# Optimization experiments

Measured on AMD Instinct MI355X. Metric: run time of the kernel, lower is better.

The kernel has to match this reference:

```python
import jax, jax.numpy as jnp
import numpy as np

ALPHA = 0.2  # LeakyReLU negative slope
MASK_VAL = -9e15


def setup_inputs() -> dict:
    key = jax.random.key(0)
    k1, k2, k3 = jax.random.split(key, 3)
    bs, N, d = 16, 1024, 128
    h = jax.random.normal(k1, (bs, N, d), dtype=jnp.float32)
    # nn.Linear(in, out, bias=False).weight has shape [out, in]
    W = jax.random.normal(k2, (d, d), dtype=jnp.float32) * (1.414 / np.sqrt(d))
    # a: Linear(2*out, 1) -> weight [1, 2d] flattened to [2d], bias [1]
    a_w = jax.random.normal(k3, (2 * d,), dtype=jnp.float32) * 0.1
    a_b = jnp.zeros((1,), dtype=jnp.float32)
    return {"h": h, "W": W, "a_w": a_w, "a_b": a_b}


def reference(h, W, a_w, a_b):
    # h: [bs, N, d], W: [d, d] (torch Linear weight), a_w: [2d], a_b: [1]
    bs, N, d = h.shape
    Wh = jnp.einsum('bnd,fd->bnf', h, W)  # [bs, N, d]
    # Decompose a([Wh_i ; Wh_j]) = Wh_i . a1 + Wh_j . a2 + b  (avoids O(N^2 * 2d) concat)
    a1, a2 = a_w[:d], a_w[d:]
    s1 = Wh @ a1  # [bs, N] -- source-node contribution (row index i)
    s2 = Wh @ a2  # [bs, N] -- target-node contribution (col index j)
    e = jax.nn.leaky_relu(s1[:, :, None] + s2[:, None, :] + a_b[0], negative_slope=ALPHA)
    # adj = ones - eye: mask out the diagonal (self-edges)
    diag = jnp.eye(N, dtype=bool)
    e = jnp.where(diag[None, :, :], MASK_VAL, e)
    attention = jax.nn.softmax(e, axis=-1)  # [bs, N, N]
    h_prime = jnp.einsum('bij,bjf->bif', attention, Wh)
    return jax.nn.elu(h_prime)  # concat=True applies ELU
```

## Files before the change

### kernel.cpp

```cpp
#include <hip/hip_runtime.h>
#include <hip/hip_bf16.h>
#include <stdint.h>

#define LOG2E 1.4426950408889634f

typedef float f32x4 __attribute__((ext_vector_type(4)));
typedef short s16x8 __attribute__((ext_vector_type(8)));
typedef int   i32x4 __attribute__((ext_vector_type(4)));

__device__ __forceinline__ float bf2f(uint16_t u) {
    uint32_t x = ((uint32_t)u) << 16;
    float f;
    __builtin_memcpy(&f, &x, 4);
    return f;
}
__device__ __forceinline__ uint16_t f2bf(float f) {
    uint32_t x;
    __builtin_memcpy(&x, &f, 4);
    uint32_t r = (x + 0x7fffu + ((x >> 16) & 1u)) >> 16;
    return (uint16_t)r;
}

__global__ __launch_bounds__(256) void k0_splitW(
    const float* __restrict__ W, uint16_t* __restrict__ whi, uint16_t* __restrict__ wlo)
{
    int i = blockIdx.x * 256 + threadIdx.x;
    float x = W[i];
    uint16_t hb = f2bf(x);
    whi[i] = hb;
    wlo[i] = f2bf(x - bf2f(hb));
}

__global__ __launch_bounds__(256) void k1_gemm(
    const float* __restrict__ h, const uint16_t* __restrict__ whi_,
    const uint16_t* __restrict__ wlo_,
    const float* __restrict__ aw, const float* __restrict__ ab,
    uint16_t* __restrict__ whB, float* __restrict__ s1b,
    float* __restrict__ E1g, float* __restrict__ E2g,
    float* __restrict__ smaxrg)
{
    __shared__ float sred[4][16][2];
    const int tid = threadIdx.x;
    const int w = tid >> 6, lane = tid & 63;
    const int q = lane >> 4, n16 = lane & 15;
    const int R0 = blockIdx.x * 16;
    const int f0 = w * 32;

    f32x4 acc[2];
    acc[0] = 0.f; acc[1] = 0.f;

    const float* hrow = h + (size_t)(R0 + n16) * 128 + q * 8;
    const uint16_t* whbase = whi_ + (size_t)(f0 + n16) * 128 + q * 8;
    const uint16_t* wlbase = wlo_ + (size_t)(f0 + n16) * 128 + q * 8;
#pragma unroll
    for (int kc = 0; kc < 4; ++kc) {
        float4 x0 = *(const float4*)(hrow + kc * 32);
        float4 x1 = *(const float4*)(hrow + kc * 32 + 4);
        float xs[8] = {x0.x, x0.y, x0.z, x0.w, x1.x, x1.y, x1.z, x1.w};
        s16x8 ahi, alo;
#pragma unroll
        for (int t = 0; t < 8; ++t) {
            uint16_t hb = f2bf(xs[t]);
            ahi[t] = (short)hb;
            alo[t] = (short)f2bf(xs[t] - bf2f(hb));
        }
#pragma unroll
        for (int fb = 0; fb < 2; ++fb) {
            s16x8 bhi = *(const s16x8*)(whbase + fb * 16 * 128 + kc * 32);
            s16x8 blo = *(const s16x8*)(wlbase + fb * 16 * 128 + kc * 32);
            acc[fb] = __builtin_amdgcn_mfma_f32_16x16x32_bf16(ahi, bhi, acc[fb], 0, 0, 0);
            acc[fb] = __builtin_amdgcn_mfma_f32_16x16x32_bf16(alo, bhi, acc[fb], 0, 0, 0);
            acc[fb] = __builtin_amdgcn_mfma_f32_16x16x32_bf16(ahi, blo, acc[fb], 0, 0, 0);
        }
    }

    float s1p[4] = {0.f, 0.f, 0.f, 0.f}, s2p[4] = {0.f, 0.f, 0.f, 0.f};
#pragma unroll
    for (int fb = 0; fb < 2; ++fb) {
        float a1 = aw[f0 + fb * 16 + n16];
        float a2 = aw[128 + f0 + fb * 16 + n16];
#pragma unroll
        for (int reg = 0; reg < 4; ++reg) {
            s1p[reg] = fmaf(acc[fb][reg], a1, s1p[reg]);
            s2p[reg] = fmaf(acc[fb][reg], a2, s2p[reg]);
        }
    }
#pragma unroll
    for (int off = 1; off < 16; off <<= 1) {
#pragma unroll
        for (int reg = 0; reg < 4; ++reg) {
            s1p[reg] += __shfl_xor(s1p[reg], off);
            s2p[reg] += __shfl_xor(s2p[reg], off);
        }
    }
    if (n16 == 0) {
#pragma unroll
        for (int reg = 0; reg < 4; ++reg) {
            sred[w][q * 4 + reg][0] = s1p[reg];
            sred[w][q * 4 + reg][1] = s2p[reg];
        }
    }
    __syncthreads();
    if (tid < 16) {
        float s1 = sred[0][tid][0] + sred[1][tid][0] + sred[2][tid][0] + sred[3][tid][0];
        float s2 = sred[0][tid][1] + sred[1][tid][1] + sred[2][tid][1] + sred[3][tid][1];
        int R = R0 + tid;
        s1b[R] = LOG2E * (s1 + ab[0]);
        float s2s = LOG2E * s2;
        E1g[R] = __builtin_amdgcn_exp2f(s2s);
        E2g[R] = __builtin_amdgcn_exp2f(0.2f * s2s);
        float m = s2s;
#pragma unroll
        for (int off = 1; off < 16; off <<= 1)
            m = fmaxf(m, __shfl_xor(m, off));
        if (tid == 0) smaxrg[blockIdx.x] = m;
    }

    const int b = R0 >> 10;
    const int jt = (R0 & 1023) >> 5;
    const int rg1 = (R0 >> 4) & 1;
    uint16_t* base = whB + (size_t)b * 131072 + (size_t)jt * 512;
    const int lane8p = (rg1 * 2 + (q >> 1)) * 16 + n16;
#pragma unroll
    for (int fb = 0; fb < 2; ++fb) {
        int fblk = w * 2 + fb;
        uint32_t e0 = f2bf(acc[fb][0]), e1 = f2bf(acc[fb][1]);
        uint32_t e2 = f2bf(acc[fb][2]), e3 = f2bf(acc[fb][3]);
        uint2 val = make_uint2(e0 | (e1 << 16), e2 | (e3 << 16));
        *(uint2*)(base + fblk * 16384 + lane8p * 8 + (q & 1) * 4) = val;
    }
}

__global__ __launch_bounds__(64) void k2_attn(
    const uint16_t* __restrict__ whB, const float* __restrict__ s1b,
    const float* __restrict__ E1g, const float* __restrict__ E2g,
    const float* __restrict__ smaxrg, float* __restrict__ out)
{
    const int lane = threadIdx.x;
    const int q = lane >> 4, n16 = lane & 15;
    const int idx = blockIdx.x;
    const int xcd = idx & 7;
    const int o = idx >> 3;
    const int b = ((o >> 7) << 3) | xcd;
    const int rem = o & 127;
    const int rg = rem >> 2;
    const int fq = rem & 3;
    const int jb = b << 10;
    const int iw0 = rg * 32;
    const int f0 = fq * 32;

    float M = smaxrg[(b << 6) | lane];
#pragma unroll
    for (int off = 1; off < 64; off <<= 1)
        M = fmaxf(M, __shfl_xor(M, off));

    float eA[2], eB[2];
#pragma unroll
    for (int rf = 0; rf < 2; ++rf) {
        float s1v = s1b[jb + iw0 + rf * 16 + n16];
        float tm = s1v + M;
        float mi = fmaxf(tm, 0.2f * tm);
        eA[rf] = __builtin_amdgcn_exp2f(s1v - mi);
        eB[rf] = __builtin_amdgcn_exp2f(fmaf(0.2f, s1v, -mi));
    }

    f32x4 acc[2][2], accl[2];
#pragma unroll
    for (int rf = 0; rf < 2; ++rf) {
        acc[rf][0] = 0.f; acc[rf][1] = 0.f; accl[rf] = 0.f;
    }

    s16x8 Bones;
#pragma unroll
    for (int t = 0; t < 8; ++t) Bones[t] = (short)0x3F80;

    const uint16_t* wb = whB + ((size_t)b << 17) + lane * 8;
    const float* e1p = E1g + jb + q * 8;
    const float* e2p = E2g + jb + q * 8;
    const int fblk0 = fq * 2, fblk1 = fq * 2 + 1;

    s16x8 Bc0 = *(const s16x8*)(wb + fblk0 * 16384);
    s16x8 Bc1 = *(const s16x8*)(wb + fblk1 * 16384);
    float4 c1a = *(const float4*)(e1p);
    float4 c1b = *(const float4*)(e1p + 4);
    float4 c2a = *(const float4*)(e2p);
    float4 c2b = *(const float4*)(e2p + 4);

    for (int jt = 0; jt < 32; ++jt) {
        const int jn = (jt < 31) ? jt + 1 : 31;
        const uint16_t* bpn = wb + jn * 512;
        s16x8 Bn0 = *(const s16x8*)(bpn + fblk0 * 16384);
        s16x8 Bn1 = *(const s16x8*)(bpn + fblk1 * 16384);
        float4 n1a = *(const float4*)(e1p + jn * 32);
        float4 n1b = *(const float4*)(e1p + jn * 32 + 4);
        float4 n2a = *(const float4*)(e2p + jn * 32);
        float4 n2b = *(const float4*)(e2p + jn * 32 + 4);

        float e1v[8] = {c1a.x, c1a.y, c1a.z, c1a.w, c1b.x, c1b.y, c1b.z, c1b.w};
        float e2v[8] = {c2a.x, c2a.y, c2a.z, c2a.w, c2b.x, c2b.y, c2b.z, c2b.w};

        s16x8 A[2];
#pragma unroll
        for (int rf = 0; rf < 2; ++rf) {
            i32x4 pk;
#pragma unroll
            for (int pr = 0; pr < 4; ++pr) {
                float p0 = fmaxf(eA[rf] * e1v[2 * pr],     eB[rf] * e2v[2 * pr]);
                float p1 = fmaxf(eA[rf] * e1v[2 * pr + 1], eB[rf] * e2v[2 * pr + 1]);
                pk[pr] = (int)__builtin_amdgcn_perm(
                    __builtin_bit_cast(uint32_t, p1),
                    __builtin_bit_cast(uint32_t, p0), 0x07060302u);
            }
            A[rf] = __builtin_bit_cast(s16x8, pk);
        }
#pragma unroll
        for (int rf = 0; rf < 2; ++rf) {
            acc[rf][0] = __builtin_amdgcn_mfma_f32_16x16x32_bf16(A[rf], Bc0, acc[rf][0], 0, 0, 0);
            acc[rf][1] = __builtin_amdgcn_mfma_f32_16x16x32_bf16(A[rf], Bc1, acc[rf][1], 0, 0, 0);
            accl[rf]   = __builtin_amdgcn_mfma_f32_16x16x32_bf16(A[rf], Bones, accl[rf], 0, 0, 0);
        }
        Bc0 = Bn0; Bc1 = Bn1;
        c1a = n1a; c1b = n1b; c2a = n2a; c2b = n2b;
    }

#pragma unroll
    for (int rf = 0; rf < 2; ++rf) {
#pragma unroll
        for (int reg = 0; reg < 4; ++reg) {
            int iw = iw0 + rf * 16 + q * 4 + reg;
            float s1v = s1b[jb + iw];
            float tm = s1v + M;
            float mi = fmaxf(tm, 0.2f * tm);
            float eAr = __builtin_amdgcn_exp2f(s1v - mi);
            float eBr = __builtin_amdgcn_exp2f(fmaf(0.2f, s1v, -mi));
            float p = fmaxf(eAr * E1g[jb + iw], eBr * E2g[jb + iw]);
            float pt = __builtin_bit_cast(float, __builtin_bit_cast(uint32_t, p) & 0xffff0000u);
            accl[rf][reg] -= pt;
            int lane_i = ((iw >> 3) & 3) * 16 + n16;
#pragma unroll
            for (int fb = 0; fb < 2; ++fb) {
                size_t a = ((size_t)b << 17) + (size_t)(fq * 2 + fb) * 16384 +
                           (size_t)(iw >> 5) * 512 + lane_i * 8 + (iw & 7);
                float wv = bf2f(whB[a]);
                acc[rf][fb][reg] -= pt * wv;
            }
        }
    }

#pragma unroll
    for (int rf = 0; rf < 2; ++rf) {
#pragma unroll
        for (int reg = 0; reg < 4; ++reg) {
            float rl = 1.0f / accl[rf][reg];
            int row = jb + iw0 + rf * 16 + q * 4 + reg;
#pragma unroll
            for (int fb = 0; fb < 2; ++fb) {
                float v = acc[rf][fb][reg] * rl;
                float e = v > 0.f ? v : (__builtin_amdgcn_exp2f(v * LOG2E) - 1.f);
                out[(size_t)row * 128 + f0 + fb * 16 + n16] = e;
            }
        }
    }
}

extern "C" void kernel_launch(void* const* d_in, const int* in_sizes, int n_in,
                              void* d_out, int out_size, void* d_ws, size_t ws_size,
                              hipStream_t stream) {
    (void)in_sizes; (void)n_in; (void)out_size; (void)ws_size;
    const float* h  = (const float*)d_in[0];
    const float* W  = (const float*)d_in[1];
    const float* aw = (const float*)d_in[2];
    const float* ab = (const float*)d_in[3];
    float* out = (float*)d_out;

    uint16_t* whB = (uint16_t*)d_ws;
    float* s1b    = (float*)((char*)d_ws + (4u << 20));
    float* E1g    = s1b + 16384;
    float* E2g    = E1g + 16384;
    float* smaxrg = E2g + 16384;
    uint16_t* whi = (uint16_t*)(smaxrg + 1024);
    uint16_t* wlo = whi + 16384;

    k0_splitW<<<64, 256, 0, stream>>>(W, whi, wlo);
    k1_gemm<<<1024, 256, 0, stream>>>(h, whi, wlo, aw, ab, whB, s1b, E1g, E2g, smaxrg);
    k2_attn<<<2048, 64, 0, stream>>>(whB, s1b, E1g, E2g, smaxrg, out);
}
```

Before: 94.60 us.

## Split attention j-loop across two waves with LDS reduction

The attention kernel now launches 128-thread blocks. Each of the two waves processes half of the key tiles and accumulates partial numerator and denominator MFMA results. The partials are exchanged through shared memory with a barrier, and each wave then finalizes one row-fragment (diagonal correction, normalization, ELU). The goal is to halve the per-wave serial loop and double the available waves to hide latency. The cost is extra LDS traffic, a sync, and possible scratch use from runtime-indexed accumulator arrays.

```diff
diff --git a/kernel.cpp b/kernel.cpp
--- a/kernel.cpp
+++ b/kernel.cpp
@@ -131,12 +131,15 @@
     }
 }
 
-__global__ __launch_bounds__(64) void k2_attn(
+__global__ __launch_bounds__(128, 4) void k2_attn(
     const uint16_t* __restrict__ whB, const float* __restrict__ s1b,
     const float* __restrict__ E1g, const float* __restrict__ E2g,
     const float* __restrict__ smaxrg, float* __restrict__ out)
 {
-    const int lane = threadIdx.x;
+    __shared__ float red[2][12][64];
+    const int tid = threadIdx.x;
+    const int wv = tid >> 6;
+    const int lane = tid & 63;
     const int q = lane >> 4, n16 = lane & 15;
     const int idx = blockIdx.x;
     const int xcd = idx & 7;
@@ -174,27 +177,29 @@
 #pragma unroll
     for (int t = 0; t < 8; ++t) Bones[t] = (short)0x3F80;
 
+    const int fblk0 = fq * 2, fblk1 = fq * 2 + 1;
+    const int jt0 = wv << 4;
     const uint16_t* wb = whB + ((size_t)b << 17) + lane * 8;
-    const float* e1p = E1g + jb + q * 8;
-    const float* e2p = E2g + jb + q * 8;
-    const int fblk0 = fq * 2, fblk1 = fq * 2 + 1;
-
-    s16x8 Bc0 = *(const s16x8*)(wb + fblk0 * 16384);
-    s16x8 Bc1 = *(const s16x8*)(wb + fblk1 * 16384);
-    float4 c1a = *(const float4*)(e1p);
-    float4 c1b = *(const float4*)(e1p + 4);
-    float4 c2a = *(const float4*)(e2p);
-    float4 c2b = *(const float4*)(e2p + 4);
-
-    for (int jt = 0; jt < 32; ++jt) {
-        const int jn = (jt < 31) ? jt + 1 : 31;
-        const uint16_t* bpn = wb + jn * 512;
+    const uint16_t* wb0 = wb + jt0 * 512;
+    const float* e1q = E1g + jb + jt0 * 32 + q * 8;
+    const float* e2q = E2g + jb + jt0 * 32 + q * 8;
+
+    s16x8 Bc0 = *(const s16x8*)(wb0 + fblk0 * 16384);
+    s16x8 Bc1 = *(const s16x8*)(wb0 + fblk1 * 16384);
+    float4 c1a = *(const float4*)(e1q);
+    float4 c1b = *(const float4*)(e1q + 4);
+    float4 c2a = *(const float4*)(e2q);
+    float4 c2b = *(const float4*)(e2q + 4);
+
+    for (int t = 0; t < 16; ++t) {
+        const int tn = (t < 15) ? t + 1 : 15;
+        const uint16_t* bpn = wb0 + tn * 512;
         s16x8 Bn0 = *(const s16x8*)(bpn + fblk0 * 16384);
         s16x8 Bn1 = *(const s16x8*)(bpn + fblk1 * 16384);
-        float4 n1a = *(const float4*)(e1p + jn * 32);
-        float4 n1b = *(const float4*)(e1p + jn * 32 + 4);
-        float4 n2a = *(const float4*)(e2p + jn * 32);
-        float4 n2b = *(const float4*)(e2p + jn * 32 + 4);
+        float4 n1a = *(const float4*)(e1q + tn * 32);
+        float4 n1b = *(const float4*)(e1q + tn * 32 + 4);
+        float4 n2a = *(const float4*)(e2q + tn * 32);
+        float4 n2b = *(const float4*)(e2q + tn * 32 + 4);
 
         float e1v[8] = {c1a.x, c1a.y, c1a.z, c1a.w, c1b.x, c1b.y, c1b.z, c1b.w};
         float e2v[8] = {c2a.x, c2a.y, c2a.z, c2a.w, c2b.x, c2b.y, c2b.z, c2b.w};
@@ -223,8 +228,27 @@
         c1a = n1a; c1b = n1b; c2a = n2a; c2b = n2b;
     }
 
-#pragma unroll
-    for (int rf = 0; rf < 2; ++rf) {
+    const int orf = 1 - wv;
+#pragma unroll
+    for (int fb = 0; fb < 2; ++fb)
+#pragma unroll
+        for (int reg = 0; reg < 4; ++reg)
+            red[wv][fb * 4 + reg][lane] = acc[orf][fb][reg];
+#pragma unroll
+    for (int reg = 0; reg < 4; ++reg)
+        red[wv][8 + reg][lane] = accl[orf][reg];
+    __syncthreads();
+#pragma unroll
+    for (int fb = 0; fb < 2; ++fb)
+#pragma unroll
+        for (int reg = 0; reg < 4; ++reg)
+            acc[wv][fb][reg] += red[orf][fb * 4 + reg][lane];
+#pragma unroll
+    for (int reg = 0; reg < 4; ++reg)
+        accl[wv][reg] += red[orf][8 + reg][lane];
+
+    {
+        const int rf = wv;
 #pragma unroll
         for (int reg = 0; reg < 4; ++reg) {
             int iw = iw0 + rf * 16 + q * 4 + reg;
@@ -241,14 +265,14 @@
             for (int fb = 0; fb < 2; ++fb) {
                 size_t a = ((size_t)b << 17) + (size_t)(fq * 2 + fb) * 16384 +
                            (size_t)(iw >> 5) * 512 + lane_i * 8 + (iw & 7);
-                float wv = bf2f(whB[a]);
-                acc[rf][fb][reg] -= pt * wv;
+                float wv_ = bf2f(whB[a]);
+                acc[rf][fb][reg] -= pt * wv_;
             }
         }
     }
 
-#pragma unroll
-    for (int rf = 0; rf < 2; ++rf) {
+    {
+        const int rf = wv;
 #pragma unroll
         for (int reg = 0; reg < 4; ++reg) {
             float rl = 1.0f / accl[rf][reg];
@@ -283,5 +307,5 @@
 
     k0_splitW<<<64, 256, 0, stream>>>(W, whi, wlo);
     k1_gemm<<<1024, 256, 0, stream>>>(h, whi, wlo, aw, ab, whB, s1b, E1g, E2g, smaxrg);
-    k2_attn<<<2048, 64, 0, stream>>>(whB, s1b, E1g, E2g, smaxrg, out);
-}
+    k2_attn<<<2048, 128, 0, stream>>>(whB, s1b, E1g, E2g, smaxrg, out);
+}
```

Measured after the change: 107.4 us. 13.6% more time.
